# Optimization experiments

Measured on AMD Instinct MI355X. Metric: run time of the kernel, lower is better.

Reference implementation:

```python
import jax, jax.numpy as jnp
import numpy as np

N_NODES = 50000
IN_CH = 128
HID_CH = 256
N_EDGES = 800000

def setup_inputs() -> dict:
    key = jax.random.key(0)
    k1, k2, k3, k4, k5 = jax.random.split(key, 5)
    x = jax.random.normal(k1, (N_NODES, IN_CH), dtype=jnp.float32)
    edge_index = jax.random.randint(k2, (2, N_EDGES), 0, N_NODES, dtype=jnp.int64)
    # SAGEConv params: lin_l (applied to aggregated neighbors, has bias), lin_r (applied to root, no bias)
    s = 1.0 / np.sqrt(IN_CH)
    W_l = jax.random.uniform(k3, (IN_CH, HID_CH), dtype=jnp.float32, minval=-s, maxval=s)
    b_l = jnp.zeros((HID_CH,), dtype=jnp.float32)
    W_r = jax.random.uniform(k4, (IN_CH, HID_CH), dtype=jnp.float32, minval=-s, maxval=s)
    return {"x": x, "edge_index": edge_index, "W_l": W_l, "b_l": b_l, "W_r": W_r}

def reference(x, edge_index, W_l, b_l, W_r):
    src, dst = edge_index[0], edge_index[1]
    # gather source features along edges, scatter-mean into destination nodes
    msgs = x[src]  # [E, in]
    agg_sum = jax.ops.segment_sum(msgs, dst, num_segments=N_NODES)  # [N, in]
    deg = jax.ops.segment_sum(jnp.ones((N_EDGES,), x.dtype), dst, num_segments=N_NODES)
    agg = agg_sum / jnp.maximum(deg, 1.0)[:, None]
    # SAGEConv: lin_l(aggregated) + lin_r(root), then ReLU
    out = agg @ W_l + b_l + x @ W_r
    return jax.nn.relu(out)
```

## Files before the change

kernel.cpp:

```cpp
#include <hip/hip_runtime.h>
#include <hip/hip_bf16.h>

#define IN_CH   128
#define HID_CH  256
#define KTOT    256
#define LDS_RS  72

#define BUCK_NODES 128
#define NBUCK      391
#define BUCK_CAP   2432
#define SCHUNK     4096

typedef __attribute__((ext_vector_type(8))) short bf16x8;
typedef __attribute__((ext_vector_type(4))) float f32x4;
typedef __attribute__((ext_vector_type(2))) float f32x2;

static __device__ __forceinline__ unsigned short f2bf(float f) {
    unsigned int u = __float_as_uint(f);
    unsigned int r = (u + 0x7FFFu + ((u >> 16) & 1u)) >> 16;
    return (unsigned short)r;
}
static __device__ __forceinline__ float bf2f(unsigned int ubits16) {
    return __uint_as_float(ubits16 << 16);
}

static __device__ __forceinline__ unsigned enc_e4m3(float f) {
    unsigned u = __float_as_uint(f);
    unsigned s = (u >> 24) & 0x80u;
    float af = fabsf(f);
    if (af >= 448.f) return s | 0x7Eu;
    if (af < 0.0009765625f) return s;
    if (af < 0.015625f) {
        int m = (int)(af * 512.0f + 0.5f);
        if (m > 7) return s | 0x08u;
        return s | (unsigned)m;
    }
    unsigned au = u & 0x7fffffffu;
    unsigned r = au + 0x0007FFFFu + ((au >> 20) & 1u);
    unsigned e8 = r >> 23;
    unsigned m = (r >> 20) & 7u;
    int e4 = (int)e8 - 120;
    if (e4 >= 16) return s | 0x7Eu;
    return s | ((unsigned)e4 << 3) | m;
}

static __device__ __forceinline__ void dec4_e4m3(unsigned v, float& c0, float& c1,
                                                 float& c2, float& c3) {
#if __has_builtin(__builtin_amdgcn_cvt_pk_f32_fp8)
    f32x2 dlo = __builtin_amdgcn_cvt_pk_f32_fp8(v, false);
    f32x2 dhi = __builtin_amdgcn_cvt_pk_f32_fp8(v, true);
    c0 = dlo.x; c1 = dlo.y; c2 = dhi.x; c3 = dhi.y;
#else
    unsigned b[4] = {v & 0xFFu, (v >> 8) & 0xFFu, (v >> 16) & 0xFFu, v >> 24};
    float o[4];
    #pragma unroll
    for (int i = 0; i < 4; ++i) {
        unsigned e = (b[i] >> 3) & 15u, m = b[i] & 7u;
        unsigned nz = (e != 0u) ? 1u : 0u;
        float val = (float)(m + (nz << 3)) * __uint_as_float((e + 117u + (1u - nz)) << 23);
        o[i] = (b[i] & 0x80u) ? -val : val;
    }
    c0 = o[0]; c1 = o[1]; c2 = o[2]; c3 = o[3];
#endif
}

__global__ __launch_bounds__(1024) void front_kernel(
    const float* __restrict__ x, const int* __restrict__ ei,
    const float* __restrict__ Wl, const float* __restrict__ Wr,
    unsigned short* __restrict__ featb, unsigned char* __restrict__ fx8,
    unsigned short* __restrict__ WT, int* __restrict__ histg,
    int N, int Npad, int E, int nchunk, int nxb)
{
    __shared__ int h[NBUCK];
    const int b = blockIdx.x, tid = threadIdx.x;

    if (b < 64) {
        int t = b * 1024 + tid;
        int n = t >> 8, k = t & 255;
        float v = (k < IN_CH) ? Wl[(size_t)k * HID_CH + n]
                              : Wr[(size_t)(k - IN_CH) * HID_CH + n];
        WT[(size_t)n * KTOT + k] = f2bf(v);
        return;
    }
    if (b < 64 + nxb) {
        int t = (b - 64) * 1024 + tid;
        if (t >= Npad * 16) return;
        int n = t >> 4, c8 = (t & 15) * 8;
        if (n >= N) {
            uint4 z = {0u, 0u, 0u, 0u};
            *reinterpret_cast<uint4*>(featb + (size_t)n * KTOT + c8) = z;
            *reinterpret_cast<uint4*>(featb + (size_t)n * KTOT + IN_CH + c8) = z;
            uint2 z2 = {0u, 0u};
            *reinterpret_cast<uint2*>(fx8 + (size_t)n * IN_CH + c8) = z2;
            return;
        }
        const float* src = x + (size_t)n * IN_CH + c8;
        float4 v0 = *reinterpret_cast<const float4*>(src);
        float4 v1 = *reinterpret_cast<const float4*>(src + 4);
        uint4 o;
        o.x = (unsigned)f2bf(v0.x) | ((unsigned)f2bf(v0.y) << 16);
        o.y = (unsigned)f2bf(v0.z) | ((unsigned)f2bf(v0.w) << 16);
        o.z = (unsigned)f2bf(v1.x) | ((unsigned)f2bf(v1.y) << 16);
        o.w = (unsigned)f2bf(v1.z) | ((unsigned)f2bf(v1.w) << 16);
        *reinterpret_cast<uint4*>(featb + (size_t)n * KTOT + IN_CH + c8) = o;
        uint2 p;
        p.x = enc_e4m3(v0.x) | (enc_e4m3(v0.y) << 8) |
              (enc_e4m3(v0.z) << 16) | (enc_e4m3(v0.w) << 24);
        p.y = enc_e4m3(v1.x) | (enc_e4m3(v1.y) << 8) |
              (enc_e4m3(v1.z) << 16) | (enc_e4m3(v1.w) << 24);
        *reinterpret_cast<uint2*>(fx8 + (size_t)n * IN_CH + c8) = p;
        return;
    }
    int c = b - 64 - nxb;
    if (tid < NBUCK) h[tid] = 0;
    __syncthreads();
    #pragma unroll
    for (int r = 0; r < SCHUNK / 1024; ++r) {
        int i = c * SCHUNK + r * 1024 + tid;
        if (i < E) atomicAdd(&h[((unsigned)ei[E + i]) >> 7], 1);
    }
    __syncthreads();
    if (tid < NBUCK) histg[(size_t)tid * nchunk + c] = h[tid];
}

__global__ __launch_bounds__(1024) void rowscan_kernel(
    int* __restrict__ histg, int* __restrict__ btot, int nchunk)
{
    __shared__ int s[1024];
    const int b = blockIdx.x, t = threadIdx.x;
    int v = (t < nchunk) ? histg[(size_t)b * nchunk + t] : 0;
    s[t] = v;
    __syncthreads();
    #pragma unroll
    for (int off = 1; off < 1024; off <<= 1) {
        int add = (t >= off) ? s[t - off] : 0;
        __syncthreads();
        s[t] += add;
        __syncthreads();
    }
    if (t < nchunk) histg[(size_t)b * nchunk + t] = s[t] - v;
    if (t == 1023) btot[b] = s[1023];
}

__global__ __launch_bounds__(1024) void scatter_part_kernel(
    const int* __restrict__ ei, const int* __restrict__ histg,
    const int* __restrict__ btot, unsigned* __restrict__ barr,
    int E, int nchunk)
{
    __shared__ unsigned stagr[SCHUNK];
    __shared__ unsigned stag[SCHUNK];
    __shared__ unsigned short bidr[SCHUNK];
    __shared__ unsigned short bid[SCHUNK];
    __shared__ int lh[NBUCK];
    __shared__ int lstart[NBUCK];
    __shared__ int lc[NBUCK];
    __shared__ int ls[512];
    __shared__ int sb[512];

    const int c = blockIdx.x, tid = threadIdx.x;
    const int e0 = c * SCHUNK;
    const int nval = min(SCHUNK, E - e0);

    if (tid < NBUCK) lh[tid] = 0;
    if (tid < 512) sb[tid] = (tid < NBUCK) ? btot[tid] : 0;
    __syncthreads();

    #pragma unroll
    for (int r = 0; r < SCHUNK / 1024; ++r) {
        int li = r * 1024 + tid;
        if (li < nval) {
            int i = e0 + li;
            unsigned src = (unsigned)ei[i];
            unsigned dst = (unsigned)ei[E + i];
            unsigned bkt = dst >> 7;
            stagr[li] = src | ((dst & 127u) << 16);
            bidr[li] = (unsigned short)bkt;
            atomicAdd(&lh[bkt], 1);
        }
    }
    __syncthreads();
    #pragma unroll
    for (int off = 1; off < 512; off <<= 1) {
        int add = (tid < 512 && tid >= off) ? sb[tid - off] : 0;
        __syncthreads();
        if (tid < 512) sb[tid] += add;
        __syncthreads();
    }
    if (tid < 512) ls[tid] = (tid < NBUCK) ? lh[tid] : 0;
    __syncthreads();
    #pragma unroll
    for (int off = 1; off < 512; off <<= 1) {
        int add = (tid < 512 && tid >= off) ? ls[tid - off] : 0;
        __syncthreads();
        if (tid < 512) ls[tid] += add;
        __syncthreads();
    }
    if (tid < NBUCK) {
        int st = ls[tid] - lh[tid];
        lstart[tid] = st;
        lc[tid] = 0;
    }
    __syncthreads();

    #pragma unroll
    for (int r = 0; r < SCHUNK / 1024; ++r) {
        int li = r * 1024 + tid;
        if (li < nval) {
            unsigned bkt = bidr[li];
            int pos = lstart[bkt] + atomicAdd(&lc[bkt], 1);
            stag[pos] = stagr[li];
            bid[pos] = (unsigned short)bkt;
        }
    }
    __syncthreads();

    #pragma unroll
    for (int r = 0; r < SCHUNK / 1024; ++r) {
        int li = r * 1024 + tid;
        if (li < nval) {
            unsigned bkt = bid[li];
            int gbase = histg[(size_t)bkt * nchunk + c] +
                        ((bkt == 0) ? 0 : sb[bkt - 1]);
            barr[(size_t)gbase + (li - lstart[bkt])] = stag[li];
        }
    }
}

__global__ __launch_bounds__(1024) void fused_gather_kernel(
    const unsigned* __restrict__ barr, const int* __restrict__ btot,
    const unsigned char* __restrict__ fx8, unsigned short* __restrict__ featb,
    int N)
{
    __shared__ unsigned s_edge[BUCK_CAP];
    __shared__ unsigned short s_col[BUCK_CAP];
    __shared__ int s_cnt[BUCK_NODES];
    __shared__ int s_start[BUCK_NODES];
    __shared__ int s_cur[BUCK_NODES];
    __shared__ int s_scan[BUCK_NODES];
    __shared__ int sb[512];

    const int b = blockIdx.x;
    const int tid = threadIdx.x;
    const int node0 = b * BUCK_NODES;
    const int nnodes = min(BUCK_NODES, N - node0);

    if (tid < 512) sb[tid] = (tid < NBUCK) ? btot[tid] : 0;
    if (tid < BUCK_NODES) s_cnt[tid] = 0;
    __syncthreads();
    #pragma unroll
    for (int off = 1; off < 512; off <<= 1) {
        int add = (tid < 512 && tid >= off) ? sb[tid - off] : 0;
        __syncthreads();
        if (tid < 512) sb[tid] += add;
        __syncthreads();
    }
    const int base = (b == 0) ? 0 : sb[b - 1];
    int nb = btot[b];
    nb = (nb < BUCK_CAP) ? nb : BUCK_CAP;

    for (int i = tid; i < nb; i += 1024) {
        unsigned p = barr[(size_t)base + i];
        s_edge[i] = p;
        atomicAdd(&s_cnt[p >> 16], 1);
    }
    __syncthreads();

    if (tid < BUCK_NODES) s_scan[tid] = s_cnt[tid];
    __syncthreads();
    #pragma unroll
    for (int off = 1; off < BUCK_NODES; off <<= 1) {
        int add = 0;
        if (tid < BUCK_NODES && tid >= off) add = s_scan[tid - off];
        __syncthreads();
        if (tid < BUCK_NODES) s_scan[tid] += add;
        __syncthreads();
    }
    if (tid < BUCK_NODES) {
        int st = s_scan[tid] - s_cnt[tid];
        s_start[tid] = st;
        s_cur[tid] = st;
    }
    __syncthreads();

    for (int i = tid; i < nb; i += 1024) {
        unsigned p = s_edge[i];
        int pos = atomicAdd(&s_cur[p >> 16], 1);
        s_col[pos] = (unsigned short)(p & 0xFFFFu);
    }
    __syncthreads();

    const int wid = tid >> 6, lane = tid & 63;
    const int half = lane >> 5, sub = lane & 31;
    for (int pr = wid; pr < BUCK_NODES / 2; pr += 16) {
        int ln = pr * 2 + half;
        bool live = (ln < nnodes);
        int deg = live ? s_cnt[ln] : 0;
        int beg = live ? s_start[ln] : 0;
        float a0 = 0.f, a1 = 0.f, a2 = 0.f, a3 = 0.f;
        for (int e = 0; e < deg; e += 8) {
            unsigned vv[8];
            #pragma unroll
            for (int q = 0; q < 8; ++q) {
                int ee = e + q;
                ee = (ee < deg) ? ee : (deg - 1);
                int s = s_col[beg + ee];
                vv[q] = *reinterpret_cast<const unsigned*>(
                    fx8 + (size_t)s * IN_CH + sub * 4);
            }
            #pragma unroll
            for (int q = 0; q < 8; ++q) {
                float m = (e + q < deg) ? 1.f : 0.f;
                float c0, c1, c2, c3;
                dec4_e4m3(vv[q], c0, c1, c2, c3);
                a0 = fmaf(m, c0, a0); a1 = fmaf(m, c1, a1);
                a2 = fmaf(m, c2, a2); a3 = fmaf(m, c3, a3);
            }
        }
        if (live) {
            float inv = 1.0f / fmaxf((float)deg, 1.0f);
            uint2 o;
            o.x = (unsigned)f2bf(a0 * inv) | ((unsigned)f2bf(a1 * inv) << 16);
            o.y = (unsigned)f2bf(a2 * inv) | ((unsigned)f2bf(a3 * inv) << 16);
            *reinterpret_cast<uint2*>(
                featb + (size_t)(node0 + ln) * KTOT + sub * 4) = o;
        }
    }
}

__global__ __launch_bounds__(256, 2) void sage_mfma_kernel(
    const unsigned short* __restrict__ featb,
    const unsigned short* __restrict__ WT,
    const float* __restrict__ bl,
    float* __restrict__ out, int N)
{
    __shared__ unsigned short sA[128][LDS_RS];
    __shared__ unsigned short sB[256][LDS_RS];

    const int tid   = threadIdx.x;
    const int nbase = blockIdx.x * 128;
    const int lane  = tid & 63;
    const int w     = tid >> 6;
    const int wr    = (w >> 1) * 64;
    const int wc    = (w & 1) * 128;
    const int lr    = lane & 15;
    const int lk    = (lane >> 4) * 8;

    f32x4 acc[4][8] = {};

    for (int kb = 0; kb < KTOT; kb += 64) {
        __syncthreads();
        #pragma unroll
        for (int p = 0; p < 4; ++p) {
            int c = tid + p * 256;
            int row = c >> 3, q = c & 7;
            uint4 va = *reinterpret_cast<const uint4*>(
                featb + (size_t)(nbase + row) * KTOT + kb + q * 8);
            *reinterpret_cast<uint4*>(&sA[row][q * 8]) = va;
        }
        #pragma unroll
        for (int p = 0; p < 8; ++p) {
            int c = tid + p * 256;
            int row = c >> 3, q = c & 7;
            uint4 vb = *reinterpret_cast<const uint4*>(
                WT + (size_t)row * KTOT + kb + q * 8);
            *reinterpret_cast<uint4*>(&sB[row][q * 8]) = vb;
        }
        __syncthreads();
        #pragma unroll
        for (int ks = 0; ks < 2; ++ks) {
            bf16x8 af[4], bfr[8];
            #pragma unroll
            for (int i = 0; i < 4; ++i)
                af[i] = *reinterpret_cast<const bf16x8*>(&sA[wr + i * 16 + lr][ks * 32 + lk]);
            #pragma unroll
            for (int i = 0; i < 8; ++i)
                bfr[i] = *reinterpret_cast<const bf16x8*>(&sB[wc + i * 16 + lr][ks * 32 + lk]);
            #pragma unroll
            for (int mi = 0; mi < 4; ++mi)
                #pragma unroll
                for (int ni = 0; ni < 8; ++ni)
                    acc[mi][ni] = __builtin_amdgcn_mfma_f32_16x16x32_bf16(
                        af[mi], bfr[ni], acc[mi][ni], 0, 0, 0);
        }
    }

    #pragma unroll
    for (int ni = 0; ni < 8; ++ni) {
        float bias = bl[wc + ni * 16 + lr];
        #pragma unroll
        for (int mi = 0; mi < 4; ++mi) {
            #pragma unroll
            for (int r = 0; r < 4; ++r) {
                int row = nbase + wr + mi * 16 + (lane >> 4) * 4 + r;
                if (row < N) {
                    int colj = wc + ni * 16 + lr;
                    out[(size_t)row * HID_CH + colj] = fmaxf(acc[mi][ni][r] + bias, 0.0f);
                }
            }
        }
    }
}

extern "C" void kernel_launch(void* const* d_in, const int* in_sizes, int n_in,
                              void* d_out, int out_size, void* d_ws, size_t ws_size,
                              hipStream_t stream) {
    const float* x  = (const float*)d_in[0];
    const int*   ei = (const int*)d_in[1];
    const float* Wl = (const float*)d_in[2];
    const float* bl = (const float*)d_in[3];
    const float* Wr = (const float*)d_in[4];
    float* out = (float*)d_out;

    const int N = in_sizes[0] / IN_CH;
    const int E = in_sizes[1] / 2;
    const int Npad   = ((N + 127) / 128) * 128;
    const int nchunk = (E + SCHUNK - 1) / SCHUNK;
    const int nxb    = (Npad * 16 + 1023) / 1024;

    unsigned short* featb = (unsigned short*)d_ws;
    unsigned short* WT    = featb + (size_t)Npad * KTOT;
    unsigned char*  fx8   = (unsigned char*)(WT + KTOT * HID_CH);
    unsigned* barr = (unsigned*)(fx8 + (size_t)Npad * IN_CH);
    int* histg = (int*)(barr + E);
    int* btot  = histg + (size_t)NBUCK * nchunk;

    front_kernel<<<64 + nxb + nchunk, 1024, 0, stream>>>(
        x, ei, Wl, Wr, featb, fx8, WT, histg, N, Npad, E, nchunk, nxb);
    rowscan_kernel<<<NBUCK, 1024, 0, stream>>>(histg, btot, nchunk);
    scatter_part_kernel<<<nchunk, 1024, 0, stream>>>(ei, histg, btot, barr, E, nchunk);
    fused_gather_kernel<<<NBUCK, 1024, 0, stream>>>(barr, btot, fx8, featb, N);
    sage_mfma_kernel<<<Npad / 128, 256, 0, stream>>>(featb, WT, bl, out, N);
}
```

Before: 82.84 us.

## Use direct global-to-LDS loads in GEMM and widen aggregation gathers

The GEMM kernel's tile staging now uses global_load_lds 16-byte transfers straight into shared memory, skipping the register round trip. The shared arrays lose their padding, which may bring LDS bank conflicts on the MFMA fragment reads. The aggregation kernel now processes four nodes per wavefront with 16 lanes each, loading 8 fp8 values per lane. This halves the gather instruction count and widens the bf16 store, at the cost of more accumulator registers.

```diff
diff --git a/kernel.cpp b/kernel.cpp
--- a/kernel.cpp
+++ b/kernel.cpp
@@ -4,7 +4,6 @@
 #define IN_CH   128
 #define HID_CH  256
 #define KTOT    256
-#define LDS_RS  72
 
 #define BUCK_NODES 128
 #define NBUCK      391
@@ -22,6 +21,12 @@
 }
 static __device__ __forceinline__ float bf2f(unsigned int ubits16) {
     return __uint_as_float(ubits16 << 16);
+}
+
+static __device__ __forceinline__ void gload_lds16(const void* g, void* l) {
+    __builtin_amdgcn_global_load_lds(
+        (const __attribute__((address_space(1))) void*)g,
+        (__attribute__((address_space(3))) void*)l, 16, 0, 0);
 }
 
 static __device__ __forceinline__ unsigned enc_e4m3(float f) {
@@ -290,39 +295,45 @@
     __syncthreads();
 
     const int wid = tid >> 6, lane = tid & 63;
-    const int half = lane >> 5, sub = lane & 31;
-    for (int pr = wid; pr < BUCK_NODES / 2; pr += 16) {
-        int ln = pr * 2 + half;
+    const int q4 = lane >> 4, sub = lane & 15;
+    for (int pr = wid; pr < BUCK_NODES / 4; pr += 16) {
+        int ln = pr * 4 + q4;
         bool live = (ln < nnodes);
         int deg = live ? s_cnt[ln] : 0;
         int beg = live ? s_start[ln] : 0;
         float a0 = 0.f, a1 = 0.f, a2 = 0.f, a3 = 0.f;
+        float a4 = 0.f, a5 = 0.f, a6 = 0.f, a7 = 0.f;
         for (int e = 0; e < deg; e += 8) {
-            unsigned vv[8];
+            uint2 vv[8];
             #pragma unroll
             for (int q = 0; q < 8; ++q) {
                 int ee = e + q;
                 ee = (ee < deg) ? ee : (deg - 1);
                 int s = s_col[beg + ee];
-                vv[q] = *reinterpret_cast<const unsigned*>(
-                    fx8 + (size_t)s * IN_CH + sub * 4);
+                vv[q] = *reinterpret_cast<const uint2*>(
+                    fx8 + (size_t)s * IN_CH + sub * 8);
             }
             #pragma unroll
             for (int q = 0; q < 8; ++q) {
                 float m = (e + q < deg) ? 1.f : 0.f;
-                float c0, c1, c2, c3;
-                dec4_e4m3(vv[q], c0, c1, c2, c3);
+                float c0, c1, c2, c3, c4, c5, c6, c7;
+                dec4_e4m3(vv[q].x, c0, c1, c2, c3);
+                dec4_e4m3(vv[q].y, c4, c5, c6, c7);
                 a0 = fmaf(m, c0, a0); a1 = fmaf(m, c1, a1);
                 a2 = fmaf(m, c2, a2); a3 = fmaf(m, c3, a3);
+                a4 = fmaf(m, c4, a4); a5 = fmaf(m, c5, a5);
+                a6 = fmaf(m, c6, a6); a7 = fmaf(m, c7, a7);
             }
         }
         if (live) {
             float inv = 1.0f / fmaxf((float)deg, 1.0f);
-            uint2 o;
+            uint4 o;
             o.x = (unsigned)f2bf(a0 * inv) | ((unsigned)f2bf(a1 * inv) << 16);
             o.y = (unsigned)f2bf(a2 * inv) | ((unsigned)f2bf(a3 * inv) << 16);
-            *reinterpret_cast<uint2*>(
-                featb + (size_t)(node0 + ln) * KTOT + sub * 4) = o;
+            o.z = (unsigned)f2bf(a4 * inv) | ((unsigned)f2bf(a5 * inv) << 16);
+            o.w = (unsigned)f2bf(a6 * inv) | ((unsigned)f2bf(a7 * inv) << 16);
+            *reinterpret_cast<uint4*>(
+                featb + (size_t)(node0 + ln) * KTOT + sub * 8) = o;
         }
     }
 }
@@ -333,8 +344,8 @@
     const float* __restrict__ bl,
     float* __restrict__ out, int N)
 {
-    __shared__ unsigned short sA[128][LDS_RS];
-    __shared__ unsigned short sB[256][LDS_RS];
+    __shared__ unsigned short sA[128][64];
+    __shared__ unsigned short sB[256][64];
 
     const int tid   = threadIdx.x;
     const int nbase = blockIdx.x * 128;
@@ -344,6 +355,8 @@
     const int wc    = (w & 1) * 128;
     const int lr    = lane & 15;
     const int lk    = (lane >> 4) * 8;
+    const int srow  = lane >> 3;
+    const int scol  = (lane & 7) * 8;
 
     f32x4 acc[4][8] = {};
 
@@ -351,19 +364,15 @@
         __syncthreads();
         #pragma unroll
         for (int p = 0; p < 4; ++p) {
-            int c = tid + p * 256;
-            int row = c >> 3, q = c & 7;
-            uint4 va = *reinterpret_cast<const uint4*>(
-                featb + (size_t)(nbase + row) * KTOT + kb + q * 8);
-            *reinterpret_cast<uint4*>(&sA[row][q * 8]) = va;
+            int r0 = (w + p * 4) * 8;
+            gload_lds16(featb + (size_t)(nbase + r0 + srow) * KTOT + kb + scol,
+                        &sA[r0][0]);
         }
         #pragma unroll
         for (int p = 0; p < 8; ++p) {
-            int c = tid + p * 256;
-            int row = c >> 3, q = c & 7;
-            uint4 vb = *reinterpret_cast<const uint4*>(
-                WT + (size_t)row * KTOT + kb + q * 8);
-            *reinterpret_cast<uint4*>(&sB[row][q * 8]) = vb;
+            int r0 = (w + p * 4) * 8;
+            gload_lds16(WT + (size_t)(r0 + srow) * KTOT + kb + scol,
+                        &sB[r0][0]);
         }
         __syncthreads();
         #pragma unroll
```

Result: faster. 79.90 us (-3.5%).
